# Kernel optimization log

Hardware: AMD Instinct MI355X
Metric: run time of the kernel (lower is better)

Reference implementation:

```python
import jax, jax.numpy as jnp
import numpy as np

HEADS = 8
LOCAL_ATTN_CTX = 64  # local_attn_ctx
BLOCKSIZE = 32       # only used for divisibility assert in original


def _strided_transpose(x, local_attn_ctx):
    # [n, t, e] -> group seq into (bT_ctx, local) blocks and transpose them
    n, t, e = x.shape
    bT_ctx = t // local_attn_ctx
    x = x.reshape(n, bT_ctx, local_attn_ctx, e)
    x = jnp.transpose(x, (0, 2, 1, 3))
    return x.reshape(n, t, e)


def setup_inputs() -> dict:
    key = jax.random.key(0)
    kq, kk, kv = jax.random.split(key, 3)
    shape = (4, 4096, 512)  # [batch, n_ctx, embd]
    return {
        "q": jax.random.normal(kq, shape, dtype=jnp.float32),
        "k": jax.random.normal(kk, shape, dtype=jnp.float32),
        "v": jax.random.normal(kv, shape, dtype=jnp.float32),
    }


def reference(q, k, v):
    n_ctx = q.shape[1]
    bT_ctx = n_ctx // LOCAL_ATTN_CTX
    assert bT_ctx % BLOCKSIZE == 0
    # strided permutation of the sequence axis
    qs = _strided_transpose(q, LOCAL_ATTN_CTX)
    ks = _strided_transpose(k, LOCAL_ATTN_CTX)
    vs = _strided_transpose(v, LOCAL_ATTN_CTX)
    n_state = q.shape[-1] // HEADS
    scale = np.float32(1.0 / np.sqrt(n_state))
    # full attention over the permuted sequence (as in the torch impl)
    w = jnp.einsum('nte,nse->nts', qs, ks)          # [n, t, t]
    w = jax.nn.softmax(w * scale, axis=-1)
    a = jnp.einsum('nts,nse->nte', w, vs)           # [n, t, e]
    # inverse strided regrouping
    n, t, e = a.shape
    a = a.reshape(n, LOCAL_ATTN_CTX, bT_ctx, e)
    a = jnp.transpose(a, (0, 2, 1, 3))
    return a.reshape(n, t, e)
```

## Files before the change

### kernel.cpp

```cpp
#include <hip/hip_runtime.h>


typedef _Float16 half8 __attribute__((ext_vector_type(8)));
typedef float f32x16 __attribute__((ext_vector_type(16)));
typedef float f32x4v __attribute__((ext_vector_type(4)));

#define B 4
#define S 4096
#define D 512
#define QT 64
#define KT 64
#define NT 64
#define NELEM (B * S * D)

#define QSCALE 0.18033688011112042f
#define M0 20.0f

__global__ __launch_bounds__(256) void cvt(const float* __restrict__ k,
                                           const float* __restrict__ v,
                                           _Float16* __restrict__ k16,
                                           _Float16* __restrict__ v16) {
  __shared__ half8 tile[32][65];
  const int tid = threadIdx.x;
  int bx = blockIdx.x;
  if (bx < 512) {
    const int b = bx >> 7;
    const int t0 = (bx & 127) * 32;
#pragma unroll
    for (int p = 0; p < 8; ++p) {
      const int tl = p * 4 + (tid >> 6);
      const int dcl = tid & 63;
      const float* src = k + ((size_t)(b * S + t0 + tl) * D) + dcl * 8;
      f32x4v x = *(const f32x4v*)src;
      f32x4v y = *(const f32x4v*)(src + 4);
      half8 h;
      h[0] = (_Float16)x[0]; h[1] = (_Float16)x[1]; h[2] = (_Float16)x[2]; h[3] = (_Float16)x[3];
      h[4] = (_Float16)y[0]; h[5] = (_Float16)y[1]; h[6] = (_Float16)y[2]; h[7] = (_Float16)y[3];
      tile[tl][dcl] = h;
    }
    __syncthreads();
#pragma unroll
    for (int p = 0; p < 8; ++p) {
      const int dcw = p * 8 + (tid >> 5);
      const int tw = tid & 31;
      ((half8*)k16)[(size_t)(b * 64 + dcw) * S + t0 + tw] = tile[tw][dcw];
    }
  } else {
    bx -= 512;
    const int i = bx * 256 + tid;
    const int dq = i & 127;
    const int bt8 = i >> 7;
    const int b = bt8 >> 9, t8 = bt8 & 511;
    const float* src = v + ((size_t)(b * S + t8 * 8) * D) + dq * 4;
    f32x4v r[8];
#pragma unroll
    for (int j = 0; j < 8; ++j) r[j] = *(const f32x4v*)(src + (size_t)j * D);
    half8* dst = (half8*)v16 + ((size_t)bt8 * 512 + dq * 4);
#pragma unroll
    for (int c = 0; c < 4; ++c) {
      half8 h;
#pragma unroll
      for (int j = 0; j < 8; ++j) h[j] = (_Float16)r[j][c];
      dst[c] = h;
    }
  }
}

#define PBUF_H 5120
#define PBUF_OFF 0
#define LBUF_OFF (2 * PBUF_H * 2)
#define SMEM_SZ  (LBUF_OFF + 512)

__global__ __launch_bounds__(512)
__attribute__((amdgpu_waves_per_eu(2, 2)))
void attn(const float* __restrict__ q,
          const _Float16* __restrict__ k16,
          const _Float16* __restrict__ v16,
          float* __restrict__ out) {
  __shared__ __align__(16) char smem[SMEM_SZ];
  _Float16* Pbuf = (_Float16*)(smem + PBUF_OFF);
  float*    Lbuf = (float*)(smem + LBUF_OFF);

  const int tid = threadIdx.x;
  const int w = tid >> 6, lane = tid & 63;
  const int m32 = lane & 31, hi = lane >> 5;

  const int bx = blockIdx.x;
  const int xc = bx & 7, rr0 = bx >> 3;
  const int b = xc >> 1;
  const int qt = ((xc & 1) << 5) + rr0;

  if (w < 4) {
    const int rg = w & 1, kh = (w >> 1) & 1;
    const int qrow0 = qt * QT + rg * 32;

    const _Float16* kb = k16 + ((size_t)(b * 64 + hi) * S + kh * 32 + m32) * 8;
    half8 kg[2][8];
#pragma unroll
    for (int i = 0; i < 8; ++i)
      kg[0][i] = *(const half8*)(kb + (size_t)i * (S * 16));

    half8 qf[32];
    {
      const float* qb = q + ((size_t)(b * S + qrow0 + m32) * D) + hi * 8;
#pragma unroll
      for (int ks = 0; ks < 32; ++ks) {
        f32x4v x = *(const f32x4v*)(qb + ks * 16);
        f32x4v y = *(const f32x4v*)(qb + ks * 16 + 4);
        half8 h;
        h[0] = (_Float16)(x[0] * QSCALE); h[1] = (_Float16)(x[1] * QSCALE);
        h[2] = (_Float16)(x[2] * QSCALE); h[3] = (_Float16)(x[3] * QSCALE);
        h[4] = (_Float16)(y[0] * QSCALE); h[5] = (_Float16)(y[1] * QSCALE);
        h[6] = (_Float16)(y[2] * QSCALE); h[7] = (_Float16)(y[3] * QSCALE);
        qf[ks] = h;
      }
    }
    float lacc[16];
#pragma unroll
    for (int r = 0; r < 16; ++r) lacc[r] = 0.f;

    for (int t = 0; t <= NT; ++t) {
      asm volatile("s_waitcnt lgkmcnt(0)" ::: "memory");
      __builtin_amdgcn_s_barrier();
      asm volatile("" ::: "memory");
      if (t == NT) break;
      f32x16 sa0 = {}, sa1 = {};
#pragma unroll
      for (int g = 0; g < 4; ++g) {
        if (g < 3) {
#pragma unroll
          for (int i = 0; i < 8; ++i)
            kg[(g + 1) & 1][i] = *(const half8*)(kb + (size_t)((g + 1) * 8 + i) * (S * 16) +
                                                 (size_t)t * 512);
        } else if (t + 1 < NT) {
#pragma unroll
          for (int i = 0; i < 8; ++i)
            kg[0][i] = *(const half8*)(kb + (size_t)i * (S * 16) + (size_t)(t + 1) * 512);
        }
        __builtin_amdgcn_s_setprio(1);
#pragma unroll
        for (int i = 0; i < 8; i += 2) {
          sa0 = __builtin_amdgcn_mfma_f32_32x32x16_f16(qf[g * 8 + i], kg[g & 1][i], sa0, 0, 0, 0);
          sa1 = __builtin_amdgcn_mfma_f32_32x32x16_f16(qf[g * 8 + i + 1], kg[g & 1][i + 1], sa1, 0, 0, 0);
        }
        __builtin_amdgcn_s_setprio(0);
      }
      _Float16* pq = &Pbuf[(t & 1) * PBUF_H + (kh * 2 + rg) * 1280];
#pragma unroll
      for (int r = 0; r < 16; ++r) {
        float p = __builtin_amdgcn_exp2f(fminf((sa0[r] + sa1[r]) - M0, 15.0f));
        lacc[r] += p;
        const int row = (r & 3) + 8 * (r >> 2) + 4 * hi;
        pq[row * 40 + m32] = (_Float16)p;
      }
    }

#pragma unroll
    for (int r = 0; r < 16; ++r) {
      float vv = lacc[r];
      vv += __shfl_xor(vv, 1);  vv += __shfl_xor(vv, 2);
      vv += __shfl_xor(vv, 4);  vv += __shfl_xor(vv, 8);
      vv += __shfl_xor(vv, 16);
      lacc[r] = vv;
    }
    if (m32 == 0) {
#pragma unroll
      for (int r = 0; r < 16; ++r) {
        const int row = (r & 3) + 8 * (r >> 2) + 4 * hi;
        Lbuf[kh * 64 + rg * 32 + row] = lacc[r];
      }
    }
    asm volatile("s_waitcnt lgkmcnt(0)" ::: "memory");
    __builtin_amdgcn_s_barrier();
  } else {
    const int j = w - 4;
    f32x16 o[2][4];
#pragma unroll
    for (int rt = 0; rt < 2; ++rt)
#pragma unroll
      for (int dn = 0; dn < 4; ++dn) o[rt][dn] = (f32x16){};

    half8 vf[2][4];
    const _Float16* vb0 = v16 + ((size_t)(b * 512 + hi) * 512 + j * 128 + m32) * 8;

    for (int t = 0; t <= NT; ++t) {
      asm volatile("" ::: "memory");
      __builtin_amdgcn_s_barrier();
      asm volatile("" ::: "memory");
      if (t == 0) {
#pragma unroll
        for (int ks = 0; ks < 4; ++ks)
          vf[0][ks] = *(const half8*)(vb0 + ((size_t)(ks * 2) * 512) * 8);
        continue;
      }
      const int u = t - 1;

      const _Float16* pb = &Pbuf[(u & 1) * PBUF_H];
      half8 pf[2][4];
#pragma unroll
      for (int rt = 0; rt < 2; ++rt)
#pragma unroll
        for (int ks = 0; ks < 4; ++ks)
          pf[rt][ks] = *(const half8*)(pb + ((ks >> 1) * 2 + rt) * 1280 + m32 * 40 +
                                       (ks & 1) * 16 + hi * 8);

      const _Float16* vb = vb0 + (size_t)u * 8 * 512 * 8;
#pragma unroll
      for (int dn = 0; dn < 4; ++dn) {
        if (dn < 3) {
#pragma unroll
          for (int ks = 0; ks < 4; ++ks)
            vf[(dn + 1) & 1][ks] =
                *(const half8*)(vb + ((size_t)(ks * 2) * 512 + (dn + 1) * 32) * 8);
        } else if (u + 1 < NT) {
#pragma unroll
          for (int ks = 0; ks < 4; ++ks)
            vf[0][ks] = *(const half8*)(vb + ((size_t)(ks * 2 + 8) * 512) * 8);
        }
        __builtin_amdgcn_s_setprio(1);
#pragma unroll
        for (int ks = 0; ks < 4; ++ks) {
          o[0][dn] = __builtin_amdgcn_mfma_f32_32x32x16_f16(pf[0][ks], vf[dn & 1][ks],
                                                            o[0][dn], 0, 0, 0);
          o[1][dn] = __builtin_amdgcn_mfma_f32_32x32x16_f16(pf[1][ks], vf[dn & 1][ks],
                                                            o[1][dn], 0, 0, 0);
        }
        __builtin_amdgcn_s_setprio(0);
      }
    }

    asm volatile("" ::: "memory");
    __builtin_amdgcn_s_barrier();
    asm volatile("" ::: "memory");
    float* ob = out + (size_t)(b * S + qt * QT) * D + j * 128;
#pragma unroll
    for (int rt = 0; rt < 2; ++rt)
#pragma unroll
      for (int r = 0; r < 16; ++r) {
        const int row = rt * 32 + (r & 3) + 8 * (r >> 2) + 4 * hi;
        const float lt = Lbuf[row] + Lbuf[64 + row];
        const float inv = 1.0f / lt;
#pragma unroll
        for (int dn = 0; dn < 4; ++dn)
          ob[(size_t)row * D + dn * 32 + m32] = o[rt][dn][r] * inv;
      }
  }
}

extern "C" void kernel_launch(void* const* d_in, const int* in_sizes, int n_in,
                              void* d_out, int out_size, void* d_ws, size_t ws_size,
                              hipStream_t stream) {
  const float* q = (const float*)d_in[0];
  const float* k = (const float*)d_in[1];
  const float* v = (const float*)d_in[2];
  float* out = (float*)d_out;

  _Float16* k16 = (_Float16*)d_ws;
  _Float16* v16 = k16 + NELEM;

  cvt<<<1536, 256, 0, stream>>>(k, v, k16, v16);
  attn<<<256, 512, 0, stream>>>(q, k16, v16, out);
}
```

Measured before the change: 289.8 us.

## Split attention block into 16 waves with D-halved QK and shared-memory score reduction

Doubles the workgroup to 1024 threads (16 waves). The QK^T waves now split the embedding dimension in two: one half writes partial scores to a new shared buffer and the other half adds them in and does the exp/sum. The PV waves each cover half as many output columns. The aim is more waves per CU to hide latency, with fewer registers per wave. The cost is extra barriers per tile and LDS traffic for the partial-score reduction.

```diff
diff --git a/kernel.cpp b/kernel.cpp
--- a/kernel.cpp
+++ b/kernel.cpp
@@ -9,7 +9,6 @@
 #define S 4096
 #define D 512
 #define QT 64
-#define KT 64
 #define NT 64
 #define NELEM (B * S * D)
 
@@ -68,17 +67,19 @@
 
 #define PBUF_H 5120
 #define PBUF_OFF 0
-#define LBUF_OFF (2 * PBUF_H * 2)
+#define SRED_OFF (2 * PBUF_H * 2)
+#define LBUF_OFF (SRED_OFF + 16384)
 #define SMEM_SZ  (LBUF_OFF + 512)
 
-__global__ __launch_bounds__(512)
-__attribute__((amdgpu_waves_per_eu(2, 2)))
+__global__ __launch_bounds__(1024, 4)
+__attribute__((amdgpu_waves_per_eu(4, 4)))
 void attn(const float* __restrict__ q,
           const _Float16* __restrict__ k16,
           const _Float16* __restrict__ v16,
           float* __restrict__ out) {
   __shared__ __align__(16) char smem[SMEM_SZ];
   _Float16* Pbuf = (_Float16*)(smem + PBUF_OFF);
+  float*    Sred = (float*)(smem + SRED_OFF);
   float*    Lbuf = (float*)(smem + LBUF_OFF);
 
   const int tid = threadIdx.x;
@@ -90,21 +91,21 @@
   const int b = xc >> 1;
   const int qt = ((xc & 1) << 5) + rr0;
 
-  if (w < 4) {
-    const int rg = w & 1, kh = (w >> 1) & 1;
+  if (w < 8) {
+    const int rg = w & 1, kh = (w >> 1) & 1, dh = (w >> 2) & 1;
     const int qrow0 = qt * QT + rg * 32;
 
-    const _Float16* kb = k16 + ((size_t)(b * 64 + hi) * S + kh * 32 + m32) * 8;
-    half8 kg[2][8];
-#pragma unroll
-    for (int i = 0; i < 8; ++i)
+    const _Float16* kb = k16 + ((size_t)(b * 64 + dh * 32 + hi) * S + kh * 32 + m32) * 8;
+    half8 kg[2][2];
+#pragma unroll
+    for (int i = 0; i < 2; ++i)
       kg[0][i] = *(const half8*)(kb + (size_t)i * (S * 16));
 
-    half8 qf[32];
+    half8 qf[16];
     {
-      const float* qb = q + ((size_t)(b * S + qrow0 + m32) * D) + hi * 8;
-#pragma unroll
-      for (int ks = 0; ks < 32; ++ks) {
+      const float* qb = q + ((size_t)(b * S + qrow0 + m32) * D) + dh * 256 + hi * 8;
+#pragma unroll
+      for (int ks = 0; ks < 16; ++ks) {
         f32x4v x = *(const f32x4v*)(qb + ks * 16);
         f32x4v y = *(const f32x4v*)(qb + ks * 16 + 4);
         half8 h;
@@ -115,124 +116,169 @@
         qf[ks] = h;
       }
     }
-    float lacc[16];
-#pragma unroll
-    for (int r = 0; r < 16; ++r) lacc[r] = 0.f;
-
-    for (int t = 0; t <= NT; ++t) {
+    float* sredq = Sred + (kh * 2 + rg) * 1024 + lane * 4;
+
+    if (dh == 1) {
+      for (int t = 0; t <= NT; ++t) {
+        asm volatile("" ::: "memory");
+        __builtin_amdgcn_s_barrier();
+        asm volatile("" ::: "memory");
+        if (t == NT) break;
+        f32x16 sa = {};
+#pragma unroll
+        for (int g = 0; g < 8; ++g) {
+          if (g < 7) {
+#pragma unroll
+            for (int i = 0; i < 2; ++i)
+              kg[(g + 1) & 1][i] = *(const half8*)(kb + (size_t)((g + 1) * 2 + i) * (S * 16) +
+                                                   (size_t)t * 512);
+          } else if (t + 1 < NT) {
+#pragma unroll
+            for (int i = 0; i < 2; ++i)
+              kg[0][i] = *(const half8*)(kb + (size_t)i * (S * 16) + (size_t)(t + 1) * 512);
+          }
+          __builtin_amdgcn_s_setprio(1);
+          sa = __builtin_amdgcn_mfma_f32_32x32x16_f16(qf[g * 2], kg[g & 1][0], sa, 0, 0, 0);
+          sa = __builtin_amdgcn_mfma_f32_32x32x16_f16(qf[g * 2 + 1], kg[g & 1][1], sa, 0, 0, 0);
+          __builtin_amdgcn_s_setprio(0);
+        }
+#pragma unroll
+        for (int rq = 0; rq < 4; ++rq) {
+          f32x4v x = {sa[rq * 4 + 0], sa[rq * 4 + 1], sa[rq * 4 + 2], sa[rq * 4 + 3]};
+          *(f32x4v*)(sredq + rq * 256) = x;
+        }
+        asm volatile("s_waitcnt lgkmcnt(0)" ::: "memory");
+        __builtin_amdgcn_s_barrier();
+        asm volatile("" ::: "memory");
+      }
+      asm volatile("" ::: "memory");
+      __builtin_amdgcn_s_barrier();
+    } else {
+      float lacc[16];
+#pragma unroll
+      for (int r = 0; r < 16; ++r) lacc[r] = 0.f;
+
+      for (int t = 0; t <= NT; ++t) {
+        asm volatile("s_waitcnt lgkmcnt(0)" ::: "memory");
+        __builtin_amdgcn_s_barrier();
+        asm volatile("" ::: "memory");
+        if (t == NT) break;
+        f32x16 sa = {};
+#pragma unroll
+        for (int g = 0; g < 8; ++g) {
+          if (g < 7) {
+#pragma unroll
+            for (int i = 0; i < 2; ++i)
+              kg[(g + 1) & 1][i] = *(const half8*)(kb + (size_t)((g + 1) * 2 + i) * (S * 16) +
+                                                   (size_t)t * 512);
+          } else if (t + 1 < NT) {
+#pragma unroll
+            for (int i = 0; i < 2; ++i)
+              kg[0][i] = *(const half8*)(kb + (size_t)i * (S * 16) + (size_t)(t + 1) * 512);
+          }
+          __builtin_amdgcn_s_setprio(1);
+          sa = __builtin_amdgcn_mfma_f32_32x32x16_f16(qf[g * 2], kg[g & 1][0], sa, 0, 0, 0);
+          sa = __builtin_amdgcn_mfma_f32_32x32x16_f16(qf[g * 2 + 1], kg[g & 1][1], sa, 0, 0, 0);
+          __builtin_amdgcn_s_setprio(0);
+        }
+        asm volatile("" ::: "memory");
+        __builtin_amdgcn_s_barrier();
+        asm volatile("" ::: "memory");
+        _Float16* pq = &Pbuf[(t & 1) * PBUF_H + (kh * 2 + rg) * 1280];
+#pragma unroll
+        for (int rq = 0; rq < 4; ++rq) {
+          f32x4v x = *(const f32x4v*)(sredq + rq * 256);
+#pragma unroll
+          for (int c = 0; c < 4; ++c) {
+            const int r = rq * 4 + c;
+            float p = __builtin_amdgcn_exp2f(fminf((sa[r] + x[c]) - M0, 15.0f));
+            lacc[r] += p;
+            const int row = c + 8 * rq + 4 * hi;
+            pq[row * 40 + m32] = (_Float16)p;
+          }
+        }
+      }
+
+#pragma unroll
+      for (int r = 0; r < 16; ++r) {
+        float vv = lacc[r];
+        vv += __shfl_xor(vv, 1);  vv += __shfl_xor(vv, 2);
+        vv += __shfl_xor(vv, 4);  vv += __shfl_xor(vv, 8);
+        vv += __shfl_xor(vv, 16);
+        lacc[r] = vv;
+      }
+      if (m32 == 0) {
+#pragma unroll
+        for (int r = 0; r < 16; ++r) {
+          const int row = (r & 3) + 8 * (r >> 2) + 4 * hi;
+          Lbuf[kh * 64 + rg * 32 + row] = lacc[r];
+        }
+      }
       asm volatile("s_waitcnt lgkmcnt(0)" ::: "memory");
       __builtin_amdgcn_s_barrier();
-      asm volatile("" ::: "memory");
-      if (t == NT) break;
-      f32x16 sa0 = {}, sa1 = {};
-#pragma unroll
-      for (int g = 0; g < 4; ++g) {
-        if (g < 3) {
-#pragma unroll
-          for (int i = 0; i < 8; ++i)
-            kg[(g + 1) & 1][i] = *(const half8*)(kb + (size_t)((g + 1) * 8 + i) * (S * 16) +
-                                                 (size_t)t * 512);
-        } else if (t + 1 < NT) {
-#pragma unroll
-          for (int i = 0; i < 8; ++i)
-            kg[0][i] = *(const half8*)(kb + (size_t)i * (S * 16) + (size_t)(t + 1) * 512);
-        }
-        __builtin_amdgcn_s_setprio(1);
-#pragma unroll
-        for (int i = 0; i < 8; i += 2) {
-          sa0 = __builtin_amdgcn_mfma_f32_32x32x16_f16(qf[g * 8 + i], kg[g & 1][i], sa0, 0, 0, 0);
-          sa1 = __builtin_amdgcn_mfma_f32_32x32x16_f16(qf[g * 8 + i + 1], kg[g & 1][i + 1], sa1, 0, 0, 0);
-        }
-        __builtin_amdgcn_s_setprio(0);
-      }
-      _Float16* pq = &Pbuf[(t & 1) * PBUF_H + (kh * 2 + rg) * 1280];
-#pragma unroll
-      for (int r = 0; r < 16; ++r) {
-        float p = __builtin_amdgcn_exp2f(fminf((sa0[r] + sa1[r]) - M0, 15.0f));
-        lacc[r] += p;
-        const int row = (r & 3) + 8 * (r >> 2) + 4 * hi;
-        pq[row * 40 + m32] = (_Float16)p;
-      }
-    }
-
-#pragma unroll
-    for (int r = 0; r < 16; ++r) {
-      float vv = lacc[r];
-      vv += __shfl_xor(vv, 1);  vv += __shfl_xor(vv, 2);
-      vv += __shfl_xor(vv, 4);  vv += __shfl_xor(vv, 8);
-      vv += __shfl_xor(vv, 16);
-      lacc[r] = vv;
-    }
-    if (m32 == 0) {
-#pragma unroll
-      for (int r = 0; r < 16; ++r) {
-        const int row = (r & 3) + 8 * (r >> 2) + 4 * hi;
-        Lbuf[kh * 64 + rg * 32 + row] = lacc[r];
-      }
-    }
-    asm volatile("s_waitcnt lgkmcnt(0)" ::: "memory");
-    __builtin_amdgcn_s_barrier();
+    }
   } else {
-    const int j = w - 4;
-    f32x16 o[2][4];
+    const int j = w - 8;
+    f32x16 o[2][2];
 #pragma unroll
     for (int rt = 0; rt < 2; ++rt)
 #pragma unroll
-      for (int dn = 0; dn < 4; ++dn) o[rt][dn] = (f32x16){};
-
-    half8 vf[2][4];
-    const _Float16* vb0 = v16 + ((size_t)(b * 512 + hi) * 512 + j * 128 + m32) * 8;
+      for (int dn = 0; dn < 2; ++dn) o[rt][dn] = (f32x16){};
+
+    half8 vf[2][2], pf[2][4];
+    const _Float16* vb0 = v16 + ((size_t)(b * 512 + hi) * 512 + j * 64 + m32) * 8;
+#pragma unroll
+    for (int dn = 0; dn < 2; ++dn)
+      vf[0][dn] = *(const half8*)(vb0 + dn * 256);
 
     for (int t = 0; t <= NT; ++t) {
       asm volatile("" ::: "memory");
       __builtin_amdgcn_s_barrier();
       asm volatile("" ::: "memory");
-      if (t == 0) {
-#pragma unroll
-        for (int ks = 0; ks < 4; ++ks)
-          vf[0][ks] = *(const half8*)(vb0 + ((size_t)(ks * 2) * 512) * 8);
-        continue;
-      }
-      const int u = t - 1;
-
-      const _Float16* pb = &Pbuf[(u & 1) * PBUF_H];
-      half8 pf[2][4];
-#pragma unroll
-      for (int rt = 0; rt < 2; ++rt)
-#pragma unroll
-        for (int ks = 0; ks < 4; ++ks)
-          pf[rt][ks] = *(const half8*)(pb + ((ks >> 1) * 2 + rt) * 1280 + m32 * 40 +
-                                       (ks & 1) * 16 + hi * 8);
-
-      const _Float16* vb = vb0 + (size_t)u * 8 * 512 * 8;
-#pragma unroll
-      for (int dn = 0; dn < 4; ++dn) {
-        if (dn < 3) {
+      if (t > 0) {
+        const _Float16* pb = &Pbuf[((t - 1) & 1) * PBUF_H];
+#pragma unroll
+        for (int rt = 0; rt < 2; ++rt)
 #pragma unroll
           for (int ks = 0; ks < 4; ++ks)
-            vf[(dn + 1) & 1][ks] =
-                *(const half8*)(vb + ((size_t)(ks * 2) * 512 + (dn + 1) * 32) * 8);
-        } else if (u + 1 < NT) {
-#pragma unroll
-          for (int ks = 0; ks < 4; ++ks)
-            vf[0][ks] = *(const half8*)(vb + ((size_t)(ks * 2 + 8) * 512) * 8);
-        }
-        __builtin_amdgcn_s_setprio(1);
+            pf[rt][ks] = *(const half8*)(pb + ((ks >> 1) * 2 + rt) * 1280 + m32 * 40 +
+                                         (ks & 1) * 16 + hi * 8);
+      }
+      if (t < NT) {
+        asm volatile("" ::: "memory");
+        __builtin_amdgcn_s_barrier();
+        asm volatile("" ::: "memory");
+      }
+      if (t > 0) {
+        const int u = t - 1;
+        const _Float16* vb = vb0 + (size_t)u * 32768;
 #pragma unroll
         for (int ks = 0; ks < 4; ++ks) {
-          o[0][dn] = __builtin_amdgcn_mfma_f32_32x32x16_f16(pf[0][ks], vf[dn & 1][ks],
-                                                            o[0][dn], 0, 0, 0);
-          o[1][dn] = __builtin_amdgcn_mfma_f32_32x32x16_f16(pf[1][ks], vf[dn & 1][ks],
-                                                            o[1][dn], 0, 0, 0);
-        }
-        __builtin_amdgcn_s_setprio(0);
+          if (ks < 3) {
+#pragma unroll
+            for (int dn = 0; dn < 2; ++dn)
+              vf[(ks + 1) & 1][dn] = *(const half8*)(vb + (size_t)(ks + 1) * 8192 + dn * 256);
+          } else if (u + 1 < NT) {
+#pragma unroll
+            for (int dn = 0; dn < 2; ++dn)
+              vf[0][dn] = *(const half8*)(vb + (size_t)32768 + dn * 256);
+          }
+          __builtin_amdgcn_s_setprio(1);
+#pragma unroll
+          for (int rt = 0; rt < 2; ++rt)
+#pragma unroll
+            for (int dn = 0; dn < 2; ++dn)
+              o[rt][dn] = __builtin_amdgcn_mfma_f32_32x32x16_f16(pf[rt][ks], vf[ks & 1][dn],
+                                                                 o[rt][dn], 0, 0, 0);
+          __builtin_amdgcn_s_setprio(0);
+        }
       }
     }
 
     asm volatile("" ::: "memory");
     __builtin_amdgcn_s_barrier();
     asm volatile("" ::: "memory");
-    float* ob = out + (size_t)(b * S + qt * QT) * D + j * 128;
+    float* ob = out + (size_t)(b * S + qt * QT) * D + j * 64;
 #pragma unroll
     for (int rt = 0; rt < 2; ++rt)
 #pragma unroll
@@ -241,7 +287,7 @@
         const float lt = Lbuf[row] + Lbuf[64 + row];
         const float inv = 1.0f / lt;
 #pragma unroll
-        for (int dn = 0; dn < 4; ++dn)
+        for (int dn = 0; dn < 2; ++dn)
           ob[(size_t)row * D + dn * 32 + m32] = o[rt][dn][r] * inv;
       }
   }
@@ -259,5 +305,5 @@
   _Float16* v16 = k16 + NELEM;
 
   cvt<<<1536, 256, 0, stream>>>(k, v, k16, v16);
-  attn<<<256, 512, 0, stream>>>(q, k16, v16, out);
+  attn<<<256, 1024, 0, stream>>>(q, k16, v16, out);
 }
```

New measurement: 300.5 us. +3.7%, slower.
